# Kernel tuning notes

Measured on AMD Instinct MI355X. Metric: run time of the kernel, lower is better.

The kernel has to match this reference:

```python
import jax, jax.numpy as jnp
import numpy as np

B, S, D = 2, 2048, 1024
H = 16
HD = D // H  # 64
EPS = 1e-5
ROPE_BASE = 10000.0


def _rope_cos_sin(seq_len, head_dim, dtype):
    # inv_freq over even channel indices, standard rotate-half RoPE
    inv_freq = 1.0 / (ROPE_BASE ** (jnp.arange(0, head_dim, 2, dtype=jnp.float32) / head_dim))
    ang = jnp.arange(seq_len, dtype=jnp.float32)[:, None] * inv_freq[None, :]  # [S, HD/2]
    emb = jnp.concatenate([ang, ang], axis=-1)  # [S, HD]
    return jnp.cos(emb).astype(dtype), jnp.sin(emb).astype(dtype)


def _rotate_half(x):
    x1, x2 = jnp.split(x, 2, axis=-1)
    return jnp.concatenate([-x2, x1], axis=-1)


def setup_inputs() -> dict:
    key = jax.random.key(0)
    ks = jax.random.split(key, 5)
    std = 0.023  # default init_method: normal(mean=0, std=0.023)
    return {
        "hidden_states": jax.random.normal(ks[0], (B, S, D), dtype=jnp.float32),
        "ln_gamma": jnp.ones((D,), dtype=jnp.float32),
        "ln_beta": jnp.zeros((D,), dtype=jnp.float32),
        "qkv_weight": jax.random.normal(ks[1], (3 * D, D), dtype=jnp.float32) * std,
        "qkv_bias": jax.random.normal(ks[2], (3 * D,), dtype=jnp.float32) * std,
        "proj_weight": jax.random.normal(ks[3], (D, D), dtype=jnp.float32) * std,
        "proj_bias": jax.random.normal(ks[4], (D,), dtype=jnp.float32) * std,
    }


def reference(hidden_states, ln_gamma, ln_beta, qkv_weight, qkv_bias, proj_weight, proj_bias):
    b, s, d = hidden_states.shape
    # --- input LayerNorm ---
    mu = jnp.mean(hidden_states, axis=-1, keepdims=True)
    var = jnp.mean(jnp.square(hidden_states - mu), axis=-1, keepdims=True)
    x = (hidden_states - mu) * jax.lax.rsqrt(var + EPS) * ln_gamma + ln_beta

    # --- fused QKV projection (interleaved per-head q,k,v) ---
    qkv = x @ qkv_weight.T + qkv_bias  # [B,S,3D]
    qkv = qkv.reshape(b, s, H, 3, HD)
    q, k, v = qkv[..., 0, :], qkv[..., 1, :], qkv[..., 2, :]  # each [B,S,H,HD]

    # --- RoPE on q and k ---
    cos, sin = _rope_cos_sin(s, HD, q.dtype)  # [S,HD]
    cos = cos[None, :, None, :]
    sin = sin[None, :, None, :]
    q = q * cos + _rotate_half(q) * sin
    k = k * cos + _rotate_half(k) * sin

    # --- causal scaled-dot-product attention ---
    scale = 1.0 / jnp.sqrt(jnp.asarray(HD, dtype=q.dtype))
    scores = jnp.einsum("bqhd,bkhd->bhqk", q, k) * scale  # [B,H,S,S]
    causal = jnp.tril(jnp.ones((s, s), dtype=bool))
    scores = jnp.where(causal[None, None, :, :], scores, jnp.finfo(scores.dtype).min)
    probs = jax.nn.softmax(scores, axis=-1)
    ctx = jnp.einsum("bhqk,bkhd->bqhd", probs, v).reshape(b, s, d)

    # --- output projection ---
    return ctx @ proj_weight.T + proj_bias
```

## Files before the change

kernel.cpp:

```cpp
#include <hip/hip_runtime.h>
#include <math.h>

#define B_  2
#define S_  2048
#define D_  1024
#define H_  16
#define HD_ 64
#define BS_ (B_ * S_)

typedef __bf16 bf16_t;
typedef __bf16 bf16x8 __attribute__((ext_vector_type(8)));
typedef __bf16 bf16x4 __attribute__((ext_vector_type(4)));
typedef float  f32x4  __attribute__((ext_vector_type(4)));
typedef short  s16x4  __attribute__((ext_vector_type(4)));

#define QSCALE 0.18033688011112042f
#define FREQC  0.28782313662425575f

__device__ __forceinline__ void async_ld16(const bf16_t* g, bf16_t* l)
{
    __builtin_amdgcn_global_load_lds(
        (const __attribute__((address_space(1))) void*)g,
        (__attribute__((address_space(3))) void*)l,
        16, 0, 0);
}

__global__ __launch_bounds__(256) void cvt_w(const float* __restrict__ a,
                                             const float* __restrict__ b,
                                             bf16_t* __restrict__ oa,
                                             bf16_t* __restrict__ ob)
{
    int idx = blockIdx.x * 256 + threadIdx.x;
    const int NA = 3 * D_ * D_ / 4;
    if (idx < NA) {
        float4 v = ((const float4*)a)[idx];
        bf16x4 p;
        p[0] = (bf16_t)v.x; p[1] = (bf16_t)v.y; p[2] = (bf16_t)v.z; p[3] = (bf16_t)v.w;
        ((bf16x4*)oa)[idx] = p;
    } else {
        int j = idx - NA;
        float4 v = ((const float4*)b)[j];
        bf16x4 p;
        p[0] = (bf16_t)v.x; p[1] = (bf16_t)v.y; p[2] = (bf16_t)v.z; p[3] = (bf16_t)v.w;
        ((bf16x4*)ob)[j] = p;
    }
}

__global__ __launch_bounds__(256) void ln_kernel(const float* __restrict__ x,
                                                 const float* __restrict__ gamma,
                                                 const float* __restrict__ beta,
                                                 bf16_t* __restrict__ y)
{
    int row = blockIdx.x;
    float4 v = ((const float4*)(x + (size_t)row * D_))[threadIdx.x];
    float sum = v.x + v.y + v.z + v.w;
    float sq  = v.x * v.x + v.y * v.y + v.z * v.z + v.w * v.w;
#pragma unroll
    for (int off = 32; off > 0; off >>= 1) {
        sum += __shfl_down(sum, off);
        sq  += __shfl_down(sq, off);
    }
    __shared__ float s_sum[4], s_sq[4];
    int wave = threadIdx.x >> 6;
    if ((threadIdx.x & 63) == 0) { s_sum[wave] = sum; s_sq[wave] = sq; }
    __syncthreads();
    float tsum = s_sum[0] + s_sum[1] + s_sum[2] + s_sum[3];
    float tsq  = s_sq[0] + s_sq[1] + s_sq[2] + s_sq[3];
    float mean = tsum * (1.0f / D_);
    float var  = tsq * (1.0f / D_) - mean * mean;
    float rstd = rsqrtf(var + 1e-5f);
    float4 g = ((const float4*)gamma)[threadIdx.x];
    float4 b = ((const float4*)beta)[threadIdx.x];
    bf16x4 o;
    o[0] = (bf16_t)((v.x - mean) * rstd * g.x + b.x);
    o[1] = (bf16_t)((v.y - mean) * rstd * g.y + b.y);
    o[2] = (bf16_t)((v.z - mean) * rstd * g.z + b.z);
    o[3] = (bf16_t)((v.w - mean) * rstd * g.w + b.w);
    *(bf16x4*)&y[(size_t)row * D_ + threadIdx.x * 4] = o;
}

template<int MODE>
__global__ __launch_bounds__(256) void gemm_bf16(const bf16_t* __restrict__ A,
                                                 const bf16_t* __restrict__ W,
                                                 const float* __restrict__ bias,
                                                 float* __restrict__ outf,
                                                 bf16_t* __restrict__ qout,
                                                 bf16_t* __restrict__ kout,
                                                 bf16_t* __restrict__ vout,
                                                 int M, int N, int K)
{
    constexpr int SMEM = (MODE == 1) ? 18432 : 16384;
    __shared__ bf16_t smem[SMEM];
    const int bm = blockIdx.y * 128, bn = blockIdx.x * 128;
    const int tid = threadIdx.x;
    const int wave = tid >> 6, lane = tid & 63;
    const int ln16 = lane & 15, quad = lane >> 4;
    const int wr = (wave >> 1) * 64, wc = (wave & 1) * 64;
    const int slot_a = (quad ^ (ln16 & 3)) * 8;

    f32x4 acc[4][4];
#pragma unroll
    for (int i = 0; i < 4; i++)
#pragma unroll
        for (int j = 0; j < 4; j++) acc[i][j] = (f32x4){0.f, 0.f, 0.f, 0.f};

#pragma unroll
    for (int j = 0; j < 2; j++) {
        int e = j * 256 + tid;
        int r = e >> 2, cg = ((e & 3) ^ (r & 3)) * 8;
        async_ld16(&A[(size_t)(bm + r) * K + cg], smem + e * 8);
        async_ld16(&W[(size_t)(bn + r) * K + cg], smem + 4096 + e * 8);
    }
    __syncthreads();

    for (int k0 = 0, it = 0; k0 < K; k0 += 32, it++) {
        const bf16_t* cur = smem + (it & 1) * 8192;
        bf16_t* nxt = smem + ((it & 1) ^ 1) * 8192;
        if (k0 + 32 < K) {
#pragma unroll
            for (int j = 0; j < 2; j++) {
                int e = j * 256 + tid;
                int r = e >> 2, cg = ((e & 3) ^ (r & 3)) * 8;
                async_ld16(&A[(size_t)(bm + r) * K + k0 + 32 + cg], nxt + e * 8);
                async_ld16(&W[(size_t)(bn + r) * K + k0 + 32 + cg], nxt + 4096 + e * 8);
            }
        }

        bf16x8 af[4], bf[4];
#pragma unroll
        for (int mi = 0; mi < 4; mi++)
            af[mi] = *(const bf16x8*)&cur[(wr + mi * 16 + ln16) * 32 + slot_a];
#pragma unroll
        for (int ni = 0; ni < 4; ni++)
            bf[ni] = *(const bf16x8*)&cur[4096 + (wc + ni * 16 + ln16) * 32 + slot_a];
#pragma unroll
        for (int mi = 0; mi < 4; mi++)
#pragma unroll
            for (int ni = 0; ni < 4; ni++)
                acc[mi][ni] = __builtin_amdgcn_mfma_f32_16x16x32_bf16(
                    af[mi], bf[ni], acc[mi][ni], 0, 0, 0);

        __syncthreads();
    }

#pragma unroll
    for (int ni = 0; ni < 4; ni++) {
        float bb = bias[bn + wc + ni * 16 + ln16];
#pragma unroll
        for (int mi = 0; mi < 4; mi++)
#pragma unroll
            for (int r = 0; r < 4; r++) acc[mi][ni][r] += bb;
    }

    if (MODE == 0) {
#pragma unroll
        for (int ni = 0; ni < 4; ni++) {
            int n = bn + wc + ni * 16 + ln16;
#pragma unroll
            for (int mi = 0; mi < 4; mi++)
#pragma unroll
                for (int r = 0; r < 4; r++)
                    outf[(size_t)(bm + wr + mi * 16 + quad * 4 + r) * N + n] = acc[mi][ni][r];
        }
    } else {
        const int n64 = (bn + wc) >> 6;
        const int t = n64 % 3, h = n64 / 3;
        bf16_t* T = smem + wave * (64 * 72);
        if (t == 2) {
#pragma unroll
            for (int mi = 0; mi < 4; mi++) {
#pragma unroll
                for (int ni = 0; ni < 4; ni++) {
                    bf16x4 pk;
#pragma unroll
                    for (int r = 0; r < 4; r++) pk[r] = (bf16_t)acc[mi][ni][r];
                    *(bf16x4*)&T[(ni * 16 + ln16) * 72 + mi * 16 + quad * 4] = pk;
                }
            }
            int m0 = bm + wr;
            int bi = m0 >> 11, s0g = m0 & (S_ - 1);
#pragma unroll
            for (int e = lane; e < 512; e += 64) {
                int hd_l = e >> 3, c8 = (e & 7) << 3;
                *(bf16x8*)&vout[((size_t)(bi * H_ + h) * HD_ + hd_l) * S_ + s0g + c8] =
                    *(const bf16x8*)&T[hd_l * 72 + c8];
            }
        } else {
            float fr0 = __expf(-(float)ln16 * FREQC);
            float fr1 = __expf(-(float)(16 + ln16) * FREQC);
            float sc = (t == 0) ? QSCALE : 1.0f;
#pragma unroll
            for (int mi = 0; mi < 4; mi++) {
#pragma unroll
                for (int r = 0; r < 4; r++) {
                    int m = bm + wr + mi * 16 + quad * 4 + r;
                    float s = (float)(m & (S_ - 1));
                    float sn0, cs0, sn1, cs1;
                    __sincosf(s * fr0, &sn0, &cs0);
                    __sincosf(s * fr1, &sn1, &cs1);
                    int rowo = (mi * 16 + quad * 4 + r) * 72;
                    float x1 = acc[mi][0][r], x2 = acc[mi][2][r];
                    T[rowo + ln16]      = (bf16_t)((x1 * cs0 - x2 * sn0) * sc);
                    T[rowo + 32 + ln16] = (bf16_t)((x2 * cs0 + x1 * sn0) * sc);
                    x1 = acc[mi][1][r]; x2 = acc[mi][3][r];
                    T[rowo + 16 + ln16] = (bf16_t)((x1 * cs1 - x2 * sn1) * sc);
                    T[rowo + 48 + ln16] = (bf16_t)((x2 * cs1 + x1 * sn1) * sc);
                }
            }
            bf16_t* dst = (t == 0) ? qout : kout;
#pragma unroll
            for (int e = lane; e < 512; e += 64) {
                int row_l = e >> 3, c8 = (e & 7) << 3;
                int m = bm + wr + row_l;
                int b = m >> 11, s = m & (S_ - 1);
                *(bf16x8*)&dst[((size_t)(b * H_ + h) * S_ + s) * HD_ + c8] =
                    *(const bf16x8*)&T[row_l * 72 + c8];
            }
        }
    }
}

__global__ __launch_bounds__(256) void attn_fa(const bf16_t* __restrict__ q_buf,
                                               const bf16_t* __restrict__ k_buf,
                                               const bf16_t* __restrict__ v_t,
                                               bf16_t* __restrict__ ctx)
{
    __shared__ bf16_t KS[2][4096];
    __shared__ bf16_t VS[2][4096];

    const int bx = blockIdx.x, h = blockIdx.y, b = blockIdx.z;
    const int t = (bx < 16) ? (15 - bx) : bx;
    const int tid = threadIdx.x;
    const int wave = tid >> 6, lane = tid & 63;
    const int ln16 = lane & 15, quad = lane >> 4;
    const int w0 = t * 64 + wave * 16;
    const int ktmax = t;
    const int s7 = ln16 & 7;

    const bf16_t* qb = q_buf + (size_t)(b * H_ + h) * S_ * HD_;
    const bf16_t* kb = k_buf + (size_t)(b * H_ + h) * S_ * HD_;
    const bf16_t* vb = v_t  + (size_t)(b * H_ + h) * HD_ * S_;

    const int e0 = tid, e1 = tid + 256;
    const int r0 = e0 >> 3, c0 = ((e0 & 7) ^ (r0 & 7)) * 8;
    const int r1 = e1 >> 3, c1 = ((e1 & 7) ^ (r1 & 7)) * 8;

    bf16x8 qf[2];
#pragma unroll
    for (int kc = 0; kc < 2; kc++)
        qf[kc] = *(const bf16x8*)&qb[(size_t)(w0 + ln16) * HD_ + kc * 32 + quad * 8];

    f32x4 o[4];
#pragma unroll
    for (int mi = 0; mi < 4; mi++) o[mi] = (f32x4){0.f, 0.f, 0.f, 0.f};
    float m_i = -1e30f, l_i = 0.f;

    {
        bf16x8 ka = *(const bf16x8*)&kb[(size_t)r0 * HD_ + c0];
        bf16x8 kc_ = *(const bf16x8*)&kb[(size_t)r1 * HD_ + c1];
        bf16x8 va = *(const bf16x8*)&vb[(size_t)r0 * S_ + c0];
        bf16x8 vc = *(const bf16x8*)&vb[(size_t)r1 * S_ + c1];
        *(bf16x8*)&KS[0][e0 * 8] = ka;
        *(bf16x8*)&KS[0][e1 * 8] = kc_;
        *(bf16x8*)&VS[0][e0 * 8] = va;
        *(bf16x8*)&VS[0][e1 * 8] = vc;
    }
    int tp = (ktmax > 0) ? 1 : 0;
    bf16x8 kp0 = *(const bf16x8*)&kb[(size_t)(tp * 64 + r0) * HD_ + c0];
    bf16x8 kp1 = *(const bf16x8*)&kb[(size_t)(tp * 64 + r1) * HD_ + c1];
    bf16x8 vp0 = *(const bf16x8*)&vb[(size_t)r0 * S_ + tp * 64 + c0];
    bf16x8 vp1 = *(const bf16x8*)&vb[(size_t)r1 * S_ + tp * 64 + c1];
    __syncthreads();

    for (int kt = 0; kt <= ktmax; kt++) {
        int tn = (kt + 2 <= ktmax) ? (kt + 2) : ktmax;
        bf16x8 kn0 = *(const bf16x8*)&kb[(size_t)(tn * 64 + r0) * HD_ + c0];
        bf16x8 kn1 = *(const bf16x8*)&kb[(size_t)(tn * 64 + r1) * HD_ + c1];
        bf16x8 vn0 = *(const bf16x8*)&vb[(size_t)r0 * S_ + tn * 64 + c0];
        bf16x8 vn1 = *(const bf16x8*)&vb[(size_t)r1 * S_ + tn * 64 + c1];

        int nb = (kt + 1) & 1;
        *(bf16x8*)&KS[nb][e0 * 8] = kp0;
        *(bf16x8*)&KS[nb][e1 * 8] = kp1;
        *(bf16x8*)&VS[nb][e0 * 8] = vp0;
        *(bf16x8*)&VS[nb][e1 * 8] = vp1;

        const bf16_t* Kc = &KS[kt & 1][0];
        const bf16_t* Vc = &VS[kt & 1][0];

        f32x4 st[4];
#pragma unroll
        for (int cb = 0; cb < 4; cb++) st[cb] = (f32x4){0.f, 0.f, 0.f, 0.f};
#pragma unroll
        for (int kc = 0; kc < 2; kc++)
#pragma unroll
            for (int cb = 0; cb < 4; cb++) {
                bf16x8 kf = *(const bf16x8*)&Kc[(cb * 16 + ln16) * 64 + ((kc * 4 + quad) ^ s7) * 8];
                st[cb] = __builtin_amdgcn_mfma_f32_16x16x32_bf16(kf, qf[kc], st[cb], 0, 0, 0);
            }

        if (kt == ktmax) {
            int q_g = w0 + ln16;
#pragma unroll
            for (int cb = 0; cb < 4; cb++) {
                int key0 = kt * 64 + cb * 16 + quad * 4;
#pragma unroll
                for (int r = 0; r < 4; r++)
                    if (key0 + r > q_g) st[cb][r] = -1e30f;
            }
        }

        float mx = st[0][0];
#pragma unroll
        for (int cb = 0; cb < 4; cb++)
#pragma unroll
            for (int r = 0; r < 4; r++) mx = fmaxf(mx, st[cb][r]);
        mx = fmaxf(mx, __shfl_xor(mx, 16));
        mx = fmaxf(mx, __shfl_xor(mx, 32));
        float mn = fmaxf(m_i, mx);
        float sum = 0.f;
#pragma unroll
        for (int cb = 0; cb < 4; cb++)
#pragma unroll
            for (int r = 0; r < 4; r++) {
                float p = exp2f(st[cb][r] - mn);
                st[cb][r] = p;
                sum += p;
            }
        sum += __shfl_xor(sum, 16);
        sum += __shfl_xor(sum, 32);
        float al = exp2f(m_i - mn);
        l_i = l_i * al + sum;
        m_i = mn;
#pragma unroll
        for (int mi = 0; mi < 4; mi++) {
            o[mi][0] *= al; o[mi][1] *= al; o[mi][2] *= al; o[mi][3] *= al;
        }

        s16x4 pf4[4];
#pragma unroll
        for (int cb = 0; cb < 4; cb++) {
            union { bf16x4 hv; s16x4 sv; } u;
#pragma unroll
            for (int r = 0; r < 4; r++) u.hv[r] = (bf16_t)st[cb][r];
            pf4[cb] = u.sv;
        }

#pragma unroll
        for (int cb = 0; cb < 4; cb++) {
            int slot = ((cb * 2 + (quad >> 1)) ^ s7) * 8 + (quad & 1) * 4;
#pragma unroll
            for (int mi = 0; mi < 4; mi++) {
                union { bf16x4 hv; s16x4 sv; } uv;
                uv.hv = *(const bf16x4*)&Vc[(mi * 16 + ln16) * 64 + slot];
                o[mi] = __builtin_amdgcn_mfma_f32_16x16x16bf16_1k(uv.sv, pf4[cb], o[mi], 0, 0, 0);
            }
        }

        kp0 = kn0; kp1 = kn1; vp0 = vn0; vp1 = vn1;

        __syncthreads();
    }

    float inv = 1.0f / l_i;
    int s = w0 + ln16;
#pragma unroll
    for (int mi = 0; mi < 4; mi++) {
        bf16x4 pk;
#pragma unroll
        for (int r = 0; r < 4; r++) pk[r] = (bf16_t)(o[mi][r] * inv);
        *(bf16x4*)&ctx[(size_t)(b * S_ + s) * D_ + h * HD_ + mi * 16 + quad * 4] = pk;
    }
}

extern "C" void kernel_launch(void* const* d_in, const int* in_sizes, int n_in,
                              void* d_out, int out_size, void* d_ws, size_t ws_size,
                              hipStream_t stream)
{
    const float* hidden = (const float*)d_in[0];
    const float* gamma  = (const float*)d_in[1];
    const float* beta   = (const float*)d_in[2];
    const float* qkv_w  = (const float*)d_in[3];
    const float* qkv_b  = (const float*)d_in[4];
    const float* proj_w = (const float*)d_in[5];
    const float* proj_b = (const float*)d_in[6];
    float* out = (float*)d_out;

    char* ws = (char*)d_ws;
    const size_t MB = 1024 * 1024;
    bf16_t* x_ln = (bf16_t*)(ws);
    bf16_t* wq   = (bf16_t*)(ws +  8 * MB);
    bf16_t* wp   = (bf16_t*)(ws + 14 * MB);
    bf16_t* qbf  = (bf16_t*)(ws + 16 * MB);
    bf16_t* kbf  = (bf16_t*)(ws + 24 * MB);
    bf16_t* vtb  = (bf16_t*)(ws + 32 * MB);
    bf16_t* ctx  = (bf16_t*)(ws + 40 * MB);

    cvt_w<<<4096, 256, 0, stream>>>(qkv_w, proj_w, wq, wp);
    ln_kernel<<<BS_, 256, 0, stream>>>(hidden, gamma, beta, x_ln);
    gemm_bf16<1><<<dim3(24, 32), 256, 0, stream>>>(
        x_ln, wq, qkv_b, nullptr, qbf, kbf, vtb, BS_, 3 * D_, D_);
    attn_fa<<<dim3(32, H_, B_), 256, 0, stream>>>(qbf, kbf, vtb, ctx);
    gemm_bf16<0><<<dim3(8, 32), 256, 0, stream>>>(
        ctx, wp, proj_b, out, nullptr, nullptr, nullptr, BS_, D_, D_);
}
```

Measured before the change: 226.6 us.

## Split causal attention KV range into two chunks with separate merge kernel

The flash-attention kernel now splits the key range for query tiles at index 16 and above into two chunks of at most 16 key tiles. This launches 48 blocks per head instead of 32 and shortens the longest block's serial loop. Each block writes its unnormalized partial output plus running max and sum to workspace. A new reduction kernel merges the partials with log-sum-exp weights and writes the normalized context. The cost is one extra kernel launch and extra global traffic for the partials, and the partial outputs are rounded to bf16 before the merge.

```diff
diff --git a/kernel.cpp b/kernel.cpp
--- a/kernel.cpp
+++ b/kernel.cpp
@@ -220,21 +220,25 @@
     }
 }
 
-__global__ __launch_bounds__(256) void attn_fa(const bf16_t* __restrict__ q_buf,
+__global__ __launch_bounds__(256) void attn_p1(const bf16_t* __restrict__ q_buf,
                                                const bf16_t* __restrict__ k_buf,
                                                const bf16_t* __restrict__ v_t,
-                                               bf16_t* __restrict__ ctx)
+                                               bf16_t* __restrict__ part_o,
+                                               float* __restrict__ part_ml)
 {
     __shared__ bf16_t KS[2][4096];
     __shared__ bf16_t VS[2][4096];
 
-    const int bx = blockIdx.x, h = blockIdx.y, b = blockIdx.z;
-    const int t = (bx < 16) ? (15 - bx) : bx;
+    const int x = blockIdx.x, h = blockIdx.y, b = blockIdx.z;
+    const int t = (x < 32) ? (31 - x) : (x - 16);
+    const int c = (x < 32) ? 0 : 1;
+    const int k0c = c * 16;
+    const int k1c = min(t, k0c + 15);
+
     const int tid = threadIdx.x;
     const int wave = tid >> 6, lane = tid & 63;
     const int ln16 = lane & 15, quad = lane >> 4;
     const int w0 = t * 64 + wave * 16;
-    const int ktmax = t;
     const int s7 = ln16 & 7;
 
     const bf16_t* qb = q_buf + (size_t)(b * H_ + h) * S_ * HD_;
@@ -256,24 +260,25 @@
     float m_i = -1e30f, l_i = 0.f;
 
     {
-        bf16x8 ka = *(const bf16x8*)&kb[(size_t)r0 * HD_ + c0];
-        bf16x8 kc_ = *(const bf16x8*)&kb[(size_t)r1 * HD_ + c1];
-        bf16x8 va = *(const bf16x8*)&vb[(size_t)r0 * S_ + c0];
-        bf16x8 vc = *(const bf16x8*)&vb[(size_t)r1 * S_ + c1];
-        *(bf16x8*)&KS[0][e0 * 8] = ka;
-        *(bf16x8*)&KS[0][e1 * 8] = kc_;
-        *(bf16x8*)&VS[0][e0 * 8] = va;
-        *(bf16x8*)&VS[0][e1 * 8] = vc;
-    }
-    int tp = (ktmax > 0) ? 1 : 0;
+        bf16x8 ka = *(const bf16x8*)&kb[(size_t)(k0c * 64 + r0) * HD_ + c0];
+        bf16x8 kc_ = *(const bf16x8*)&kb[(size_t)(k0c * 64 + r1) * HD_ + c1];
+        bf16x8 va = *(const bf16x8*)&vb[(size_t)r0 * S_ + k0c * 64 + c0];
+        bf16x8 vc = *(const bf16x8*)&vb[(size_t)r1 * S_ + k0c * 64 + c1];
+        int b0 = k0c & 1;
+        *(bf16x8*)&KS[b0][e0 * 8] = ka;
+        *(bf16x8*)&KS[b0][e1 * 8] = kc_;
+        *(bf16x8*)&VS[b0][e0 * 8] = va;
+        *(bf16x8*)&VS[b0][e1 * 8] = vc;
+    }
+    int tp = (k0c + 1 <= k1c) ? (k0c + 1) : k1c;
     bf16x8 kp0 = *(const bf16x8*)&kb[(size_t)(tp * 64 + r0) * HD_ + c0];
     bf16x8 kp1 = *(const bf16x8*)&kb[(size_t)(tp * 64 + r1) * HD_ + c1];
     bf16x8 vp0 = *(const bf16x8*)&vb[(size_t)r0 * S_ + tp * 64 + c0];
     bf16x8 vp1 = *(const bf16x8*)&vb[(size_t)r1 * S_ + tp * 64 + c1];
     __syncthreads();
 
-    for (int kt = 0; kt <= ktmax; kt++) {
-        int tn = (kt + 2 <= ktmax) ? (kt + 2) : ktmax;
+    for (int kt = k0c; kt <= k1c; kt++) {
+        int tn = (kt + 2 <= k1c) ? (kt + 2) : k1c;
         bf16x8 kn0 = *(const bf16x8*)&kb[(size_t)(tn * 64 + r0) * HD_ + c0];
         bf16x8 kn1 = *(const bf16x8*)&kb[(size_t)(tn * 64 + r1) * HD_ + c1];
         bf16x8 vn0 = *(const bf16x8*)&vb[(size_t)r0 * S_ + tn * 64 + c0];
@@ -299,7 +304,7 @@
                 st[cb] = __builtin_amdgcn_mfma_f32_16x16x32_bf16(kf, qf[kc], st[cb], 0, 0, 0);
             }
 
-        if (kt == ktmax) {
+        if (kt == t) {
             int q_g = w0 + ln16;
 #pragma unroll
             for (int cb = 0; cb < 4; cb++) {
@@ -362,15 +367,65 @@
         __syncthreads();
     }
 
-    float inv = 1.0f / l_i;
-    int s = w0 + ln16;
+    const size_t pidx = (((size_t)(b * H_ + h) * 32) + t) * 2 + c;
+    bf16_t* po = part_o + pidx * 4096;
+    const int q_l = wave * 16 + ln16;
 #pragma unroll
     for (int mi = 0; mi < 4; mi++) {
         bf16x4 pk;
 #pragma unroll
-        for (int r = 0; r < 4; r++) pk[r] = (bf16_t)(o[mi][r] * inv);
-        *(bf16x4*)&ctx[(size_t)(b * S_ + s) * D_ + h * HD_ + mi * 16 + quad * 4] = pk;
-    }
+        for (int r = 0; r < 4; r++) pk[r] = (bf16_t)o[mi][r];
+        *(bf16x4*)&po[q_l * 64 + mi * 16 + quad * 4] = pk;
+    }
+    if (quad == 0) {
+        part_ml[pidx * 128 + q_l]      = m_i;
+        part_ml[pidx * 128 + 64 + q_l] = l_i;
+    }
+}
+
+__global__ __launch_bounds__(256) void attn_p2(const bf16_t* __restrict__ part_o,
+                                               const float* __restrict__ part_ml,
+                                               bf16_t* __restrict__ ctx)
+{
+    const int t = blockIdx.x, h = blockIdx.y, b = blockIdx.z;
+    const int nch = (t >> 4) + 1;
+    const size_t pidx = (((size_t)(b * H_ + h) * 32) + t) * 2;
+    const int q_l = threadIdx.x >> 2;
+    const int hg = (threadIdx.x & 3) * 16;
+
+    float m0 = part_ml[pidx * 128 + q_l];
+    float l0 = part_ml[pidx * 128 + 64 + q_l];
+    const bf16_t* o0 = part_o + pidx * 4096 + q_l * 64 + hg;
+
+    float w0, w1 = 0.f;
+    const bf16_t* o1 = o0;
+    if (nch == 2) {
+        float m1 = part_ml[(pidx + 1) * 128 + q_l];
+        float l1 = part_ml[(pidx + 1) * 128 + 64 + q_l];
+        float M = fmaxf(m0, m1);
+        float a0 = exp2f(m0 - M), a1 = exp2f(m1 - M);
+        float L = a0 * l0 + a1 * l1;
+        w0 = a0 / L; w1 = a1 / L;
+        o1 = part_o + (pidx + 1) * 4096 + q_l * 64 + hg;
+    } else {
+        w0 = 1.f / l0;
+    }
+
+    bf16x8 a0v = *(const bf16x8*)o0;
+    bf16x8 a1v = *(const bf16x8*)(o0 + 8);
+    bf16x8 b0v = *(const bf16x8*)o1;
+    bf16x8 b1v = *(const bf16x8*)(o1 + 8);
+    bf16x8 out0, out1;
+#pragma unroll
+    for (int i = 0; i < 8; i++) {
+        float f0 = (float)a0v[i] * w0 + (float)b0v[i] * w1;
+        float f1 = (float)a1v[i] * w0 + (float)b1v[i] * w1;
+        out0[i] = (bf16_t)f0;
+        out1[i] = (bf16_t)f1;
+    }
+    bf16_t* dst = &ctx[(size_t)(b * S_ + t * 64 + q_l) * D_ + h * HD_ + hg];
+    *(bf16x8*)dst = out0;
+    *(bf16x8*)(dst + 8) = out1;
 }
 
 extern "C" void kernel_launch(void* const* d_in, const int* in_sizes, int n_in,
@@ -395,12 +450,15 @@
     bf16_t* kbf  = (bf16_t*)(ws + 24 * MB);
     bf16_t* vtb  = (bf16_t*)(ws + 32 * MB);
     bf16_t* ctx  = (bf16_t*)(ws + 40 * MB);
+    bf16_t* po   = (bf16_t*)(ws + 48 * MB);
+    float*  pml  = (float*)(ws + 64 * MB);
 
     cvt_w<<<4096, 256, 0, stream>>>(qkv_w, proj_w, wq, wp);
     ln_kernel<<<BS_, 256, 0, stream>>>(hidden, gamma, beta, x_ln);
     gemm_bf16<1><<<dim3(24, 32), 256, 0, stream>>>(
         x_ln, wq, qkv_b, nullptr, qbf, kbf, vtb, BS_, 3 * D_, D_);
-    attn_fa<<<dim3(32, H_, B_), 256, 0, stream>>>(qbf, kbf, vtb, ctx);
+    attn_p1<<<dim3(48, H_, B_), 256, 0, stream>>>(qbf, kbf, vtb, po, pml);
+    attn_p2<<<dim3(32, H_, B_), 256, 0, stream>>>(po, pml, ctx);
     gemm_bf16<0><<<dim3(8, 32), 256, 0, stream>>>(
         ctx, wp, proj_b, out, nullptr, nullptr, nullptr, BS_, D_, D_);
 }
```

New measurement: 211.3 us. 6.8% less time.
